# Kernel tuning notes

Hardware: AMD Instinct MI355X
Metric: run time of the kernel (lower is better)

The kernel has to match this reference:

```python
import jax, jax.numpy as jnp
import numpy as np

N = 131072
HIDDEN = 1024
MIN_STD = 1e-5
PRIOR_SIGMA1 = 4.0 / np.sqrt(1.0)
PRIOR_SIGMA2 = 2.25 / np.sqrt(float(HIDDEN))


def setup_inputs() -> dict:
    key = jax.random.key(0)
    ks = jax.random.split(key, 13)
    f = lambda k, shape: jax.random.normal(k, shape, dtype=jnp.float32)
    return {
        "x": f(ks[0], (N, 1)),
        "W1_mu": f(ks[1], (HIDDEN, 1)),
        "W1_rho": f(ks[2], (HIDDEN, 1)),
        "b1_mu": f(ks[3], (HIDDEN,)),
        "b1_rho": f(ks[4], (HIDDEN,)),
        "W2_mu": f(ks[5], (2, HIDDEN)),
        "W2_rho": f(ks[6], (2, HIDDEN)),
        "b2_mu": f(ks[7], (2,)),
        "b2_rho": f(ks[8], (2,)),
        "eps_W1": f(ks[9], (HIDDEN, 1)),
        "eps_b1": f(ks[10], (HIDDEN,)),
        "eps_W2": f(ks[11], (2, HIDDEN)),
        "eps_b2": f(ks[12], (2,)),
    }


def _kl(mu, sigma, prior_sigma):
    # KL( N(mu, sigma) || N(0, prior_sigma) ), summed over elements
    return 0.5 * jnp.sum(
        2.0 * jnp.log(prior_sigma / sigma) - 1.0
        + (sigma / prior_sigma) ** 2
        + (mu / prior_sigma) ** 2
    )


def _bbb_linear(x, W_mu, W_rho, b_mu, b_rho, eps_W, eps_b, prior_sigma):
    W_sigma = jax.nn.softplus(W_rho)
    b_sigma = jax.nn.softplus(b_rho)
    W = W_mu + W_sigma * eps_W  # [out, in]
    b = b_mu + b_sigma * eps_b  # [out]
    out = x @ W.T + b  # [N, out]
    kl = _kl(W_mu, W_sigma, prior_sigma) + _kl(b_mu, b_sigma, prior_sigma)
    return out, kl


def reference(x, W1_mu, W1_rho, b1_mu, b1_rho, W2_mu, W2_rho, b2_mu, b2_rho,
              eps_W1, eps_b1, eps_W2, eps_b2):
    h1, kl1 = _bbb_linear(x, W1_mu, W1_rho, b1_mu, b1_rho, eps_W1, eps_b1, PRIOR_SIGMA1)
    h3, kl3 = _bbb_linear(jax.nn.relu(h1), W2_mu, W2_rho, b2_mu, b2_rho, eps_W2, eps_b2, PRIOR_SIGMA2)
    means = h3[:, 0]
    stds = MIN_STD + jax.nn.softplus(h3[:, 1])
    kl = kl1 + kl3
    return means, stds, kl
```

## Files before the change

kernel.cpp:

```cpp
#include <hip/hip_runtime.h>
#include <math.h>

#define N_SAMPLES 131072
#define HIDDEN 1024
#define SEGS 8
#define SEG_UNITS (HIDDEN / SEGS)
#define PAIRS 128
#define SAMPLES_PER_BLOCK (2 * PAIRS)

typedef float v2f __attribute__((ext_vector_type(2)));

__device__ __forceinline__ float softplusf(float v) {
    return fmaxf(v, 0.0f) + log1pf(expf(-fabsf(v)));
}
__device__ __forceinline__ float kl_term_f(float mu, float sigma, float inv_prior) {
    float r = sigma * inv_prior;
    float m = mu * inv_prior;
    return 0.5f * (-2.0f * logf(r) - 1.0f + r * r + m * m);
}

__global__ __launch_bounds__(1024) void bbb_prep(
    const float* __restrict__ W1_mu, const float* __restrict__ W1_rho,
    const float* __restrict__ b1_mu, const float* __restrict__ b1_rho,
    const float* __restrict__ W2_mu, const float* __restrict__ W2_rho,
    const float* __restrict__ b2_mu, const float* __restrict__ b2_rho,
    const float* __restrict__ eps_W1, const float* __restrict__ eps_b1,
    const float* __restrict__ eps_W2, const float* __restrict__ eps_b2,
    float4* __restrict__ params,
    float* __restrict__ kl_out)
{
    __shared__ double s_part[16];
    const int tid = threadIdx.x;

    const float ip1 = 0.25f;
    const float ip2 = 32.0f / 2.25f;

    float w1mu  = W1_mu[tid],          w1rho  = W1_rho[tid];
    float b1mu  = b1_mu[tid],          b1rho  = b1_rho[tid];
    float w2amu = W2_mu[tid],          w2arho = W2_rho[tid];
    float w2bmu = W2_mu[HIDDEN + tid], w2brho = W2_rho[HIDDEN + tid];

    float sg_w1  = softplusf(w1rho);
    float sg_b1  = softplusf(b1rho);
    float sg_w2a = softplusf(w2arho);
    float sg_w2b = softplusf(w2brho);

    float w1  = fmaf(sg_w1,  eps_W1[tid],          w1mu);
    float bb1 = fmaf(sg_b1,  eps_b1[tid],          b1mu);
    float w2a = fmaf(sg_w2a, eps_W2[tid],          w2amu);
    float w2b = fmaf(sg_w2b, eps_W2[HIDDEN + tid], w2bmu);

    params[tid] = make_float4(w1, bb1, w2a, w2b);

    double kl = (double)kl_term_f(w1mu,  sg_w1,  ip1)
              + (double)kl_term_f(b1mu,  sg_b1,  ip1)
              + (double)kl_term_f(w2amu, sg_w2a, ip2)
              + (double)kl_term_f(w2bmu, sg_w2b, ip2);

    if (tid < 2) {
        kl += (double)kl_term_f(b2_mu[tid], softplusf(b2_rho[tid]), ip2);
    }
    if (tid == 0) {
        float bb2a = fmaf(softplusf(b2_rho[0]), eps_b2[0], b2_mu[0]);
        float bb2b = fmaf(softplusf(b2_rho[1]), eps_b2[1], b2_mu[1]);
        params[HIDDEN] = make_float4(bb2a, bb2b, 0.0f, 0.0f);
    }

    #pragma unroll
    for (int off = 32; off > 0; off >>= 1) kl += __shfl_down(kl, off, 64);
    if ((tid & 63) == 0) s_part[tid >> 6] = kl;
    __syncthreads();
    if (tid == 0) {
        double t = 0.0;
        #pragma unroll
        for (int i = 0; i < 16; ++i) t += s_part[i];
        *kl_out = (float)t;
    }
}

__global__ __launch_bounds__(1024) void bbb_eval(
    const float* __restrict__ x,
    const float4* __restrict__ params,
    float* __restrict__ means,
    float* __restrict__ stds)
{
    __shared__ float4 s_part[SEGS][PAIRS];

    const int tid  = threadIdx.x;
    const int pair = tid & (PAIRS - 1);
    const int seg  = __builtin_amdgcn_readfirstlane(tid >> 7);
    const int base = blockIdx.x * SAMPLES_PER_BLOCK;

    const v2f xv = *(const v2f*)(x + base + 2 * pair);

    const float4* __restrict__ p = params + seg * SEG_UNITS;

    v2f aa = {0.0f, 0.0f};
    v2f ab = {0.0f, 0.0f};
    #pragma unroll 8
    for (int j = 0; j < SEG_UNITS; ++j) {
        float4 q = p[j];
        v2f h = __builtin_elementwise_fma((v2f)q.x, xv, (v2f)q.y);
        h = __builtin_elementwise_max(h, (v2f)0.0f);
        aa = __builtin_elementwise_fma(h, (v2f)q.z, aa);
        ab = __builtin_elementwise_fma(h, (v2f)q.w, ab);
    }
    s_part[seg][pair] = make_float4(aa.x, aa.y, ab.x, ab.y);
    __syncthreads();

    if (tid < PAIRS) {
        const float4 b2 = params[HIDDEN];
        float4 acc = s_part[0][tid];
        #pragma unroll
        for (int s = 1; s < SEGS; ++s) {
            float4 v = s_part[s][tid];
            acc.x += v.x; acc.y += v.y; acc.z += v.z; acc.w += v.w;
        }
        float m0 = acc.x + b2.x;
        float m1 = acc.y + b2.x;
        float u0 = acc.z + b2.y;
        float u1 = acc.w + b2.y;
        *(float2*)(means + base + 2 * tid) = make_float2(m0, m1);
        *(float2*)(stds  + base + 2 * tid) =
            make_float2(1e-5f + softplusf(u0), 1e-5f + softplusf(u1));
    }
}

extern "C" void kernel_launch(void* const* d_in, const int* in_sizes, int n_in,
                              void* d_out, int out_size, void* d_ws, size_t ws_size,
                              hipStream_t stream) {
    const float* x      = (const float*)d_in[0];
    const float* W1_mu  = (const float*)d_in[1];
    const float* W1_rho = (const float*)d_in[2];
    const float* b1_mu  = (const float*)d_in[3];
    const float* b1_rho = (const float*)d_in[4];
    const float* W2_mu  = (const float*)d_in[5];
    const float* W2_rho = (const float*)d_in[6];
    const float* b2_mu  = (const float*)d_in[7];
    const float* b2_rho = (const float*)d_in[8];
    const float* eps_W1 = (const float*)d_in[9];
    const float* eps_b1 = (const float*)d_in[10];
    const float* eps_W2 = (const float*)d_in[11];
    const float* eps_b2 = (const float*)d_in[12];

    float* out = (float*)d_out;
    float4* params_ws = (float4*)d_ws;

    bbb_prep<<<1, HIDDEN, 0, stream>>>(
        W1_mu, W1_rho, b1_mu, b1_rho, W2_mu, W2_rho, b2_mu, b2_rho,
        eps_W1, eps_b1, eps_W2, eps_b2,
        params_ws, out + 2 * N_SAMPLES);

    bbb_eval<<<N_SAMPLES / SAMPLES_PER_BLOCK, 1024, 0, stream>>>(
        x, params_ws, out, out + N_SAMPLES);
}
```

Measured before the change: 95.71 us.

## Replace dense hidden-layer loop with sorted breakpoint piecewise-linear lookup

Because the input is scalar, the two-layer ReLU network is a piecewise-linear function of x, with breakpoints at -b1/w1. The prep kernel now sorts the 1024 breakpoints with a bitonic sort in shared memory and prefix-sums the per-unit slope and intercept contributions into a coefficient table. The eval kernel then binary-searches each x in that table and applies one linear evaluation, replacing 1024 FMAs per sample with about ten shared-memory lookups. This puts a serial single-block sort and scan in front of the eval kernel, and summing in a different order may change the floating-point rounding compared with the direct sum.

```diff
diff --git a/kernel.cpp b/kernel.cpp
--- a/kernel.cpp
+++ b/kernel.cpp
@@ -3,12 +3,8 @@
 
 #define N_SAMPLES 131072
 #define HIDDEN 1024
-#define SEGS 8
-#define SEG_UNITS (HIDDEN / SEGS)
-#define PAIRS 128
-#define SAMPLES_PER_BLOCK (2 * PAIRS)
-
-typedef float v2f __attribute__((ext_vector_type(2)));
+#define EVAL_THREADS 256
+#define EVAL_BLOCKS (N_SAMPLES / EVAL_THREADS)
 
 __device__ __forceinline__ float softplusf(float v) {
     return fmaxf(v, 0.0f) + log1pf(expf(-fabsf(v)));
@@ -18,6 +14,10 @@
     float m = mu * inv_prior;
     return 0.5f * (-2.0f * logf(r) - 1.0f + r * r + m * m);
 }
+
+struct f4 { float x, y, z, w; };
+__device__ __forceinline__ f4 f4add(f4 a, f4 b) { return {a.x+b.x, a.y+b.y, a.z+b.z, a.w+b.w}; }
+__device__ __forceinline__ f4 f4sub(f4 a, f4 b) { return {a.x-b.x, a.y-b.y, a.z-b.z, a.w-b.w}; }
 
 __global__ __launch_bounds__(1024) void bbb_prep(
     const float* __restrict__ W1_mu, const float* __restrict__ W1_rho,
@@ -26,11 +26,21 @@
     const float* __restrict__ b2_mu, const float* __restrict__ b2_rho,
     const float* __restrict__ eps_W1, const float* __restrict__ eps_b1,
     const float* __restrict__ eps_W2, const float* __restrict__ eps_b2,
-    float4* __restrict__ params,
+    float* __restrict__ t_out,
+    float4* __restrict__ C_out,
     float* __restrict__ kl_out)
 {
+    __shared__ float  s_key[HIDDEN];
+    __shared__ int    s_idx[HIDDEN];
+    __shared__ f4     s_v[HIDDEN];
     __shared__ double s_part[16];
-    const int tid = threadIdx.x;
+    __shared__ f4     s_wtot[16];
+    __shared__ f4     s_negtot[16];
+    __shared__ float  s_b2[2];
+
+    const int tid  = threadIdx.x;
+    const int lane = tid & 63;
+    const int wid  = tid >> 6;
 
     const float ip1 = 0.25f;
     const float ip2 = 32.0f / 2.25f;
@@ -50,80 +60,138 @@
     float w2a = fmaf(sg_w2a, eps_W2[tid],          w2amu);
     float w2b = fmaf(sg_w2b, eps_W2[HIDDEN + tid], w2bmu);
 
-    params[tid] = make_float4(w1, bb1, w2a, w2b);
+    if (tid == 0) {
+        s_b2[0] = fmaf(softplusf(b2_rho[0]), eps_b2[0], b2_mu[0]);
+        s_b2[1] = fmaf(softplusf(b2_rho[1]), eps_b2[1], b2_mu[1]);
+    }
+
+    float sa = w2a * w1, ia = w2a * bb1;
+    float sb = w2b * w1, ib = w2b * bb1;
+    bool  pos = (w1 > 0.0f);
+    float t = -bb1 / w1;
+    if (w1 == 0.0f) {
+        pos = true;
+        t = (bb1 > 0.0f) ? -INFINITY : INFINITY;
+    }
+
+    f4 raw  = {sa, ia, sb, ib};
+    f4 v    = pos ? raw : f4{-sa, -ia, -sb, -ib};
+    f4 vneg = pos ? f4{0.0f, 0.0f, 0.0f, 0.0f} : raw;
+
+    s_key[tid] = t;
+    s_idx[tid] = tid;
+    s_v[tid]   = v;
 
     double kl = (double)kl_term_f(w1mu,  sg_w1,  ip1)
               + (double)kl_term_f(b1mu,  sg_b1,  ip1)
               + (double)kl_term_f(w2amu, sg_w2a, ip2)
               + (double)kl_term_f(w2bmu, sg_w2b, ip2);
-
-    if (tid < 2) {
-        kl += (double)kl_term_f(b2_mu[tid], softplusf(b2_rho[tid]), ip2);
-    }
+    if (tid < 2) kl += (double)kl_term_f(b2_mu[tid], softplusf(b2_rho[tid]), ip2);
+    #pragma unroll
+    for (int off = 32; off > 0; off >>= 1) kl += __shfl_down(kl, off, 64);
+    if (lane == 0) s_part[wid] = kl;
+
+    #pragma unroll
+    for (int off = 32; off > 0; off >>= 1) {
+        vneg.x += __shfl_down(vneg.x, off, 64);
+        vneg.y += __shfl_down(vneg.y, off, 64);
+        vneg.z += __shfl_down(vneg.z, off, 64);
+        vneg.w += __shfl_down(vneg.w, off, 64);
+    }
+    if (lane == 0) s_negtot[wid] = vneg;
+
+    __syncthreads();
+
     if (tid == 0) {
-        float bb2a = fmaf(softplusf(b2_rho[0]), eps_b2[0], b2_mu[0]);
-        float bb2b = fmaf(softplusf(b2_rho[1]), eps_b2[1], b2_mu[1]);
-        params[HIDDEN] = make_float4(bb2a, bb2b, 0.0f, 0.0f);
-    }
-
-    #pragma unroll
-    for (int off = 32; off > 0; off >>= 1) kl += __shfl_down(kl, off, 64);
-    if ((tid & 63) == 0) s_part[tid >> 6] = kl;
+        double tt = 0.0;
+        #pragma unroll
+        for (int i = 0; i < 16; ++i) tt += s_part[i];
+        *kl_out = (float)tt;
+    }
+
+    for (int k = 2; k <= HIDDEN; k <<= 1) {
+        for (int j = k >> 1; j > 0; j >>= 1) {
+            int ixj = tid ^ j;
+            if (ixj > tid) {
+                float a = s_key[tid], b = s_key[ixj];
+                bool up = ((tid & k) == 0);
+                if ((a > b) == up) {
+                    s_key[tid] = b; s_key[ixj] = a;
+                    int ti = s_idx[tid]; s_idx[tid] = s_idx[ixj]; s_idx[ixj] = ti;
+                }
+            }
+            __syncthreads();
+        }
+    }
+
+    float tkey = s_key[tid];
+    f4 vs = s_v[s_idx[tid]];
+
+    f4 tneg = s_negtot[0];
+    #pragma unroll
+    for (int i = 1; i < 16; ++i) tneg = f4add(tneg, s_negtot[i]);
+
+    f4 incl = vs;
+    #pragma unroll
+    for (int off = 1; off < 64; off <<= 1) {
+        float ax = __shfl_up(incl.x, off, 64);
+        float ay = __shfl_up(incl.y, off, 64);
+        float az = __shfl_up(incl.z, off, 64);
+        float aw = __shfl_up(incl.w, off, 64);
+        if (lane >= off) { incl.x += ax; incl.y += ay; incl.z += az; incl.w += aw; }
+    }
+    if (lane == 63) s_wtot[wid] = incl;
     __syncthreads();
-    if (tid == 0) {
-        double t = 0.0;
-        #pragma unroll
-        for (int i = 0; i < 16; ++i) t += s_part[i];
-        *kl_out = (float)t;
-    }
-}
-
-__global__ __launch_bounds__(1024) void bbb_eval(
+
+    f4 offs = {0.0f, 0.0f, 0.0f, 0.0f};
+    #pragma unroll
+    for (int w = 0; w < 16; ++w) {
+        if (w < wid) offs = f4add(offs, s_wtot[w]);
+    }
+
+    f4 excl = f4sub(f4add(offs, incl), vs);
+    f4 C = f4add(excl, tneg);
+    C.y += s_b2[0];
+    C.w += s_b2[1];
+
+    t_out[tid] = tkey;
+    C_out[tid] = make_float4(C.x, C.y, C.z, C.w);
+    if (tid == HIDDEN - 1) {
+        f4 Cl = f4add(f4add(offs, incl), tneg);
+        Cl.y += s_b2[0];
+        Cl.w += s_b2[1];
+        C_out[HIDDEN] = make_float4(Cl.x, Cl.y, Cl.z, Cl.w);
+    }
+}
+
+__global__ __launch_bounds__(EVAL_THREADS) void bbb_eval(
     const float* __restrict__ x,
-    const float4* __restrict__ params,
+    const float* __restrict__ t_sorted,
+    const float4* __restrict__ Ctab,
     float* __restrict__ means,
     float* __restrict__ stds)
 {
-    __shared__ float4 s_part[SEGS][PAIRS];
-
-    const int tid  = threadIdx.x;
-    const int pair = tid & (PAIRS - 1);
-    const int seg  = __builtin_amdgcn_readfirstlane(tid >> 7);
-    const int base = blockIdx.x * SAMPLES_PER_BLOCK;
-
-    const v2f xv = *(const v2f*)(x + base + 2 * pair);
-
-    const float4* __restrict__ p = params + seg * SEG_UNITS;
-
-    v2f aa = {0.0f, 0.0f};
-    v2f ab = {0.0f, 0.0f};
-    #pragma unroll 8
-    for (int j = 0; j < SEG_UNITS; ++j) {
-        float4 q = p[j];
-        v2f h = __builtin_elementwise_fma((v2f)q.x, xv, (v2f)q.y);
-        h = __builtin_elementwise_max(h, (v2f)0.0f);
-        aa = __builtin_elementwise_fma(h, (v2f)q.z, aa);
-        ab = __builtin_elementwise_fma(h, (v2f)q.w, ab);
-    }
-    s_part[seg][pair] = make_float4(aa.x, aa.y, ab.x, ab.y);
+    __shared__ float  s_t[HIDDEN];
+    __shared__ float4 s_C[HIDDEN + 1];
+
+    const int tid = threadIdx.x;
+    for (int i = tid; i < HIDDEN; i += EVAL_THREADS) s_t[i] = t_sorted[i];
+    for (int i = tid; i < HIDDEN + 1; i += EVAL_THREADS) s_C[i] = Ctab[i];
     __syncthreads();
 
-    if (tid < PAIRS) {
-        const float4 b2 = params[HIDDEN];
-        float4 acc = s_part[0][tid];
-        #pragma unroll
-        for (int s = 1; s < SEGS; ++s) {
-            float4 v = s_part[s][tid];
-            acc.x += v.x; acc.y += v.y; acc.z += v.z; acc.w += v.w;
-        }
-        float m0 = acc.x + b2.x;
-        float m1 = acc.y + b2.x;
-        float u0 = acc.z + b2.y;
-        float u1 = acc.w + b2.y;
-        *(float2*)(means + base + 2 * tid) = make_float2(m0, m1);
-        *(float2*)(stds  + base + 2 * tid) =
-            make_float2(1e-5f + softplusf(u0), 1e-5f + softplusf(u1));
-    }
+    const int g = blockIdx.x * EVAL_THREADS + tid;
+    const float xv = x[g];
+
+    int base = 0;
+    #pragma unroll
+    for (int half = 512; half > 0; half >>= 1) {
+        if (s_t[base + half - 1] < xv) base += half;
+    }
+    int k = base + ((s_t[base] < xv) ? 1 : 0);
+
+    float4 c = s_C[k];
+    means[g] = fmaf(c.x, xv, c.y);
+    stds[g]  = 1e-5f + softplusf(fmaf(c.z, xv, c.w));
 }
 
 extern "C" void kernel_launch(void* const* d_in, const int* in_sizes, int n_in,
@@ -144,13 +212,14 @@
     const float* eps_b2 = (const float*)d_in[12];
 
     float* out = (float*)d_out;
-    float4* params_ws = (float4*)d_ws;
+    float*  t_ws = (float*)d_ws;
+    float4* C_ws = (float4*)((char*)d_ws + 4096);
 
     bbb_prep<<<1, HIDDEN, 0, stream>>>(
         W1_mu, W1_rho, b1_mu, b1_rho, W2_mu, W2_rho, b2_mu, b2_rho,
         eps_W1, eps_b1, eps_W2, eps_b2,
-        params_ws, out + 2 * N_SAMPLES);
-
-    bbb_eval<<<N_SAMPLES / SAMPLES_PER_BLOCK, 1024, 0, stream>>>(
-        x, params_ws, out, out + N_SAMPLES);
-}
+        t_ws, C_ws, out + 2 * N_SAMPLES);
+
+    bbb_eval<<<EVAL_BLOCKS, EVAL_THREADS, 0, stream>>>(
+        x, t_ws, C_ws, out, out + N_SAMPLES);
+}
```

Measured after the change: 104.1 us. 8.8% more time.

## Fuse parameter prep into eval kernel with per-block shared-memory params

Applied to the files above, without the earlier changes.

Merges the single-block prep kernel into the eval kernel. Each of the 512 blocks now recomputes the sampled weights (softplus and fma) into LDS, and only block 0 computes the KL reduction. This drops a kernel launch and its serial dependency, and turns the inner loop's parameter reads from global/L2 loads into LDS broadcasts. In exchange every block does redundant transcendental work and reads all parameter arrays, which adds global traffic and uses more LDS per block.

```diff
diff --git a/kernel.cpp b/kernel.cpp
--- a/kernel.cpp
+++ b/kernel.cpp
@@ -7,6 +7,7 @@
 #define SEG_UNITS (HIDDEN / SEGS)
 #define PAIRS 128
 #define SAMPLES_PER_BLOCK (2 * PAIRS)
+#define BLOCKS (N_SAMPLES / SAMPLES_PER_BLOCK)
 
 typedef float v2f __attribute__((ext_vector_type(2)));
 
@@ -19,18 +20,26 @@
     return 0.5f * (-2.0f * logf(r) - 1.0f + r * r + m * m);
 }
 
-__global__ __launch_bounds__(1024) void bbb_prep(
+__global__ __launch_bounds__(1024) void bbb_fused(
+    const float* __restrict__ x,
     const float* __restrict__ W1_mu, const float* __restrict__ W1_rho,
     const float* __restrict__ b1_mu, const float* __restrict__ b1_rho,
     const float* __restrict__ W2_mu, const float* __restrict__ W2_rho,
     const float* __restrict__ b2_mu, const float* __restrict__ b2_rho,
     const float* __restrict__ eps_W1, const float* __restrict__ eps_b1,
     const float* __restrict__ eps_W2, const float* __restrict__ eps_b2,
-    float4* __restrict__ params,
+    float* __restrict__ means,
+    float* __restrict__ stds,
     float* __restrict__ kl_out)
 {
-    __shared__ double s_part[16];
-    const int tid = threadIdx.x;
+    __shared__ float4 s_params[HIDDEN];
+    __shared__ float4 s_part[SEGS][PAIRS];
+    __shared__ double s_kl[16];
+    __shared__ float  s_b2[2];
+
+    const int tid  = threadIdx.x;
+    const int lane = tid & 63;
+    const int wid  = tid >> 6;
 
     const float ip1 = 0.25f;
     const float ip2 = 32.0f / 2.25f;
@@ -50,50 +59,40 @@
     float w2a = fmaf(sg_w2a, eps_W2[tid],          w2amu);
     float w2b = fmaf(sg_w2b, eps_W2[HIDDEN + tid], w2bmu);
 
-    params[tid] = make_float4(w1, bb1, w2a, w2b);
+    s_params[tid] = make_float4(w1, bb1, w2a, w2b);
 
-    double kl = (double)kl_term_f(w1mu,  sg_w1,  ip1)
-              + (double)kl_term_f(b1mu,  sg_b1,  ip1)
-              + (double)kl_term_f(w2amu, sg_w2a, ip2)
-              + (double)kl_term_f(w2bmu, sg_w2b, ip2);
-
-    if (tid < 2) {
-        kl += (double)kl_term_f(b2_mu[tid], softplusf(b2_rho[tid]), ip2);
-    }
     if (tid == 0) {
-        float bb2a = fmaf(softplusf(b2_rho[0]), eps_b2[0], b2_mu[0]);
-        float bb2b = fmaf(softplusf(b2_rho[1]), eps_b2[1], b2_mu[1]);
-        params[HIDDEN] = make_float4(bb2a, bb2b, 0.0f, 0.0f);
+        s_b2[0] = fmaf(softplusf(b2_rho[0]), eps_b2[0], b2_mu[0]);
+        s_b2[1] = fmaf(softplusf(b2_rho[1]), eps_b2[1], b2_mu[1]);
     }
 
-    #pragma unroll
-    for (int off = 32; off > 0; off >>= 1) kl += __shfl_down(kl, off, 64);
-    if ((tid & 63) == 0) s_part[tid >> 6] = kl;
+    if (blockIdx.x == 0) {
+        double kl = (double)kl_term_f(w1mu,  sg_w1,  ip1)
+                  + (double)kl_term_f(b1mu,  sg_b1,  ip1)
+                  + (double)kl_term_f(w2amu, sg_w2a, ip2)
+                  + (double)kl_term_f(w2bmu, sg_w2b, ip2);
+        if (tid < 2) kl += (double)kl_term_f(b2_mu[tid], softplusf(b2_rho[tid]), ip2);
+        #pragma unroll
+        for (int off = 32; off > 0; off >>= 1) kl += __shfl_down(kl, off, 64);
+        if (lane == 0) s_kl[wid] = kl;
+    }
+
     __syncthreads();
-    if (tid == 0) {
+
+    if (blockIdx.x == 0 && tid == 0) {
         double t = 0.0;
         #pragma unroll
-        for (int i = 0; i < 16; ++i) t += s_part[i];
+        for (int i = 0; i < 16; ++i) t += s_kl[i];
         *kl_out = (float)t;
     }
-}
 
-__global__ __launch_bounds__(1024) void bbb_eval(
-    const float* __restrict__ x,
-    const float4* __restrict__ params,
-    float* __restrict__ means,
-    float* __restrict__ stds)
-{
-    __shared__ float4 s_part[SEGS][PAIRS];
-
-    const int tid  = threadIdx.x;
     const int pair = tid & (PAIRS - 1);
     const int seg  = __builtin_amdgcn_readfirstlane(tid >> 7);
     const int base = blockIdx.x * SAMPLES_PER_BLOCK;
 
     const v2f xv = *(const v2f*)(x + base + 2 * pair);
 
-    const float4* __restrict__ p = params + seg * SEG_UNITS;
+    const float4* p = &s_params[seg * SEG_UNITS];
 
     v2f aa = {0.0f, 0.0f};
     v2f ab = {0.0f, 0.0f};
@@ -109,17 +108,17 @@
     __syncthreads();
 
     if (tid < PAIRS) {
-        const float4 b2 = params[HIDDEN];
         float4 acc = s_part[0][tid];
         #pragma unroll
         for (int s = 1; s < SEGS; ++s) {
             float4 v = s_part[s][tid];
             acc.x += v.x; acc.y += v.y; acc.z += v.z; acc.w += v.w;
         }
-        float m0 = acc.x + b2.x;
-        float m1 = acc.y + b2.x;
-        float u0 = acc.z + b2.y;
-        float u1 = acc.w + b2.y;
+        float b2a = s_b2[0], b2b = s_b2[1];
+        float m0 = acc.x + b2a;
+        float m1 = acc.y + b2a;
+        float u0 = acc.z + b2b;
+        float u1 = acc.w + b2b;
         *(float2*)(means + base + 2 * tid) = make_float2(m0, m1);
         *(float2*)(stds  + base + 2 * tid) =
             make_float2(1e-5f + softplusf(u0), 1e-5f + softplusf(u1));
@@ -144,13 +143,10 @@
     const float* eps_b2 = (const float*)d_in[12];
 
     float* out = (float*)d_out;
-    float4* params_ws = (float4*)d_ws;
 
-    bbb_prep<<<1, HIDDEN, 0, stream>>>(
+    bbb_fused<<<BLOCKS, 1024, 0, stream>>>(
+        x,
         W1_mu, W1_rho, b1_mu, b1_rho, W2_mu, W2_rho, b2_mu, b2_rho,
         eps_W1, eps_b1, eps_W2, eps_b2,
-        params_ws, out + 2 * N_SAMPLES);
-
-    bbb_eval<<<N_SAMPLES / SAMPLES_PER_BLOCK, 1024, 0, stream>>>(
-        x, params_ws, out, out + N_SAMPLES);
+        out, out + N_SAMPLES, out + 2 * N_SAMPLES);
 }
```

New measurement: 96.66 us. No clear change (+1.0%).
